# Performance work log

Hardware: AMD Instinct MI355X
Metric: run time of the kernel (lower is better)

Reference implementation:

```python
import jax, jax.numpy as jnp
import numpy as np

B, T, D, H, DFF, E = 4, 1024, 1024, 16, 4096, 8
DH = D // H
EPS = 1e-6


def setup_inputs() -> dict:
    key = jax.random.key(0)
    ks = jax.random.split(key, 16)
    s = 0.02
    return {
        "x": jax.random.normal(ks[0], (B, T, D), jnp.float32),
        "mask": jnp.ones((B, 1, 1, T), jnp.bool_),
        "Wq": jax.random.normal(ks[1], (D, D), jnp.float32) * s,
        "bq": jnp.zeros((D,), jnp.float32),
        "Wk": jax.random.normal(ks[2], (D, D), jnp.float32) * s,
        "bk": jnp.zeros((D,), jnp.float32),
        "Wv": jax.random.normal(ks[3], (D, D), jnp.float32) * s,
        "bv": jnp.zeros((D,), jnp.float32),
        "Wo": jax.random.normal(ks[4], (D, D), jnp.float32) * s,
        "bo": jnp.zeros((D,), jnp.float32),
        "ln1_a": jnp.ones((D,), jnp.float32),
        "ln1_b": jnp.zeros((D,), jnp.float32),
        "ln2_a": jnp.ones((D,), jnp.float32),
        "ln2_b": jnp.zeros((D,), jnp.float32),
        "gW": jax.random.normal(ks[5], (D, E), jnp.float32) * s,
        "gb": jnp.zeros((E,), jnp.float32),
        "W1": jax.random.normal(ks[6], (E, D, DFF), jnp.float32) * s,
        "b1": jnp.zeros((E, DFF), jnp.float32),
        "W2": jax.random.normal(ks[7], (E, DFF, D), jnp.float32) * s,
        "b2": jnp.zeros((E, D), jnp.float32),
    }


def layer_norm(x, a, b):
    # Faithful to source: torch std is unbiased (ddof=1), divides by (std + eps)
    mean = jnp.mean(x, -1, keepdims=True)
    std = jnp.std(x, -1, keepdims=True, ddof=1)
    return a * (x - mean) / (std + EPS) + b


def mha(x, mask, Wq, bq, Wk, bk, Wv, bv, Wo, bo):
    def split(h):
        return h.reshape(B, T, H, DH).transpose(0, 2, 1, 3)  # [B,H,T,DH]
    q = split(x @ Wq + bq)
    k = split(x @ Wk + bk)
    v = split(x @ Wv + bv)
    scores = jnp.einsum("bhqd,bhkd->bhqk", q, k) / jnp.sqrt(jnp.float32(DH))
    scores = jnp.where(mask, scores, jnp.float32(-1e9))
    attn = jax.nn.softmax(scores, axis=-1)
    out = jnp.einsum("bhqk,bhkd->bhqd", attn, v)
    out = out.transpose(0, 2, 1, 3).reshape(B, T, D)
    return out @ Wo + bo


def moe(xf, gW, gb, W1, b1, W2, b2):
    # xf: [N, D] flat tokens; top-1 Switch routing
    gate_probs = jax.nn.softmax(xf @ gW + gb, axis=-1)  # [N, E]
    top1_idx = jnp.argmax(gate_probs, axis=-1)          # [N]
    top1_p = jnp.max(gate_probs, axis=-1)               # [N]
    out = jnp.zeros_like(xf)
    for e in range(E):  # fixed small structural loop over experts
        h = jax.nn.relu(xf @ W1[e] + b1[e])
        oe = h @ W2[e] + b2[e]
        sel = (top1_idx == e).astype(xf.dtype)
        out = out + (sel * top1_p)[:, None] * oe
    counts = jax.nn.one_hot(top1_idx, E, dtype=jnp.float32).sum(0)
    aux_loss = jnp.sum((counts / (B * T)) ** 2) * E
    return out, aux_loss


def reference(x, mask, Wq, bq, Wk, bk, Wv, bv, Wo, bo,
              ln1_a, ln1_b, ln2_a, ln2_b, gW, gb, W1, b1, W2, b2):
    # sublayer[0]: x + attn(norm(x))  (dropout=0, inference)
    x1 = x + mha(layer_norm(x, ln1_a, ln1_b), mask, Wq, bq, Wk, bk, Wv, bv, Wo, bo)
    # MoE applied to x1 directly (source calls feed_forward(x), not on the norm)
    ff_out, aux_loss = moe(x1.reshape(-1, D), gW, gb, W1, b1, W2, b2)
    # sublayer[1] with lambda _: ff_out  -> x1 + ff_out (norm computed but discarded)
    x2 = x1 + ff_out.reshape(B, T, D)
    return x2, aux_loss
```

## Files before the change

### kernel.cpp

```cpp
#include <hip/hip_runtime.h>

#define DEV __device__ __forceinline__

typedef unsigned short u16;
typedef __bf16 bf16x8 __attribute__((ext_vector_type(8)));
typedef float f32x4 __attribute__((ext_vector_type(4)));
typedef unsigned short us8 __attribute__((ext_vector_type(8)));

static constexpr int Bn = 4, Tn = 1024, Dn = 1024, Hn = 16, DFFn = 4096, En = 8;
static constexpr int Nn = Bn * Tn;
static constexpr int MAXT = 40;
static constexpr int HROWS = 5120;

static constexpr int MT_E = 0, MT_P0 = 40, MCNT = 80, MCUR = 88, MSEG = 96, MPERM = 112;

static constexpr size_t WQKVT_O = 0;
static constexpr size_t WOT_O   = WQKVT_O + 3ull * 1024 * 1024 * 2;
static constexpr size_t W12T_O  = WOT_O + 1ull * 1024 * 1024 * 2;
static constexpr size_t X1F_O   = W12T_O + 8ull * 1024 * 4096 * 2;
static constexpr size_t XN_O    = X1F_O + (size_t)Nn * Dn * 4;
static constexpr size_t Q_O     = XN_O + (size_t)Nn * Dn * 2;
static constexpr size_t K_O     = Q_O + (size_t)Nn * Dn * 2;
static constexpr size_t VT_O    = K_O + (size_t)Nn * Dn * 2;
static constexpr size_t X1B_O   = VT_O + (size_t)Nn * Dn * 2;
static constexpr size_t P3_O    = XN_O;
static constexpr size_t H_O     = X1B_O + (size_t)Nn * Dn * 2;
static constexpr size_t TOPP_O  = H_O + (size_t)HROWS * DFFn * 2;
static constexpr size_t TIDX_O  = TOPP_O + (size_t)Nn * 4;
static constexpr size_t META_O  = TIDX_O + (size_t)Nn * 4;

DEV u16 f2bf(float f) {
  union { float f; unsigned u; } v; v.f = f;
  unsigned r = v.u + 0x7fffu + ((v.u >> 16) & 1u);
  return (u16)(r >> 16);
}
DEV float bf2f(u16 x) {
  union { unsigned u; float f; } v; v.u = ((unsigned)x) << 16;
  return v.f;
}

DEV void gload16(const void* g, void* l) {
  __builtin_amdgcn_global_load_lds(
      (__attribute__((address_space(1))) void*)(void*)g,
      (__attribute__((address_space(3))) void*)l, 16, 0, 0);
}

DEV void sdecode64(int o, int& row, int& c) {
  row = o >> 7;
  c = ((o >> 4) & 7) ^ (row & 7);
}

DEV int aswz(int r, int c) { return c ^ (r & 7) ^ (((r >> 3) & 3) << 1); }

__global__ __launch_bounds__(256) void tcast_kernel(
    const float* __restrict__ src, u16* __restrict__ dst,
    int R, int C, long srcBatch, long dstBatch) {
  __shared__ u16 tile[64][65];
  src += (long)blockIdx.z * srcBatch;
  dst += (long)blockIdx.z * dstBatch;
  int r0 = blockIdx.y * 64, c0 = blockIdx.x * 64;
  int tr = threadIdx.x >> 4;
  int tc = (threadIdx.x & 15) * 4;
#pragma unroll
  for (int i = 0; i < 4; i++) {
    int r = tr + i * 16;
    float4 v = *reinterpret_cast<const float4*>(&src[(long)(r0 + r) * C + c0 + tc]);
    tile[r][tc + 0] = f2bf(v.x); tile[r][tc + 1] = f2bf(v.y);
    tile[r][tc + 2] = f2bf(v.z); tile[r][tc + 3] = f2bf(v.w);
  }
  __syncthreads();
#pragma unroll
  for (int i = 0; i < 4; i++) {
    int r = tr + i * 16;
    ushort4 o;
    o.x = tile[tc + 0][r]; o.y = tile[tc + 1][r];
    o.z = tile[tc + 2][r]; o.w = tile[tc + 3][r];
    *reinterpret_cast<ushort4*>(&dst[(long)(c0 + r) * R + r0 + tc]) = o;
  }
}

__global__ __launch_bounds__(256) void ln_kernel(
    const float* __restrict__ x, const float* __restrict__ a,
    const float* __restrict__ b, u16* __restrict__ xn) {
  __shared__ float red[8];
  int row = blockIdx.x, tid = threadIdx.x;
  int lane = tid & 63, w = tid >> 6;
  float4 v = *reinterpret_cast<const float4*>(&x[(size_t)row * 1024 + tid * 4]);
  float s = v.x + v.y + v.z + v.w;
  float sq = v.x * v.x + v.y * v.y + v.z * v.z + v.w * v.w;
#pragma unroll
  for (int sh = 1; sh <= 32; sh <<= 1) { s += __shfl_xor(s, sh); sq += __shfl_xor(sq, sh); }
  if (lane == 0) { red[w] = s; red[4 + w] = sq; }
  __syncthreads();
  s = red[0] + red[1] + red[2] + red[3];
  sq = red[4] + red[5] + red[6] + red[7];
  float mean = s * (1.0f / 1024.0f);
  float var = (sq - s * mean) * (1.0f / 1023.0f);
  float inv = 1.0f / (sqrtf(var) + 1e-6f);
  float4 av = *reinterpret_cast<const float4*>(&a[tid * 4]);
  float4 bv = *reinterpret_cast<const float4*>(&b[tid * 4]);
  ushort4 o;
  o.x = f2bf(av.x * (v.x - mean) * inv + bv.x);
  o.y = f2bf(av.y * (v.y - mean) * inv + bv.y);
  o.z = f2bf(av.z * (v.z - mean) * inv + bv.z);
  o.w = f2bf(av.w * (v.w - mean) * inv + bv.w);
  *reinterpret_cast<ushort4*>(&xn[(size_t)row * 1024 + tid * 4]) = o;
}

template <int MODE, int BM, int NG, int KSPLIT>
__global__ __launch_bounds__(256, 3) void gemm3_k(
    const u16* __restrict__ Ag, const u16* __restrict__ Bg,
    const float* __restrict__ f0, const float* __restrict__ f1,
    const float* __restrict__ f2, const float* __restrict__ xres,
    float* __restrict__ x1f, u16* __restrict__ ob0, u16* __restrict__ ob1,
    u16* __restrict__ ob2, u16* __restrict__ pout, const int* __restrict__ meta) {
  constexpr int K = (MODE == 3) ? 4096 : 1024;
  constexpr int KS = K / KSPLIT;
  constexpr int NSUB = KS >> 6;
  constexpr int MT = (MODE <= 1) ? (4096 / BM) : MAXT;
  constexpr int NT = (MODE == 0) ? 24 : (MODE == 2) ? 32 : 8;
  constexpr int WR = BM / 2;
  constexpr int MI = WR / 16;
  constexpr int CA = BM / 32;

  __shared__ u16 As[BM * 64];
  __shared__ u16 Bs[128 * 64];

  const int tid = threadIdx.x, lane = tid & 63, w = tid >> 6;
  const int wm = w >> 1, wn = w & 1;
  const int cL = lane >> 4, rl15 = lane & 15;

  constexpr int NWG = MT * NT * KSPLIT;
  constexpr int q8 = NWG >> 3;
  int b = blockIdx.x;
  int lg = (b & 7) * q8 + (b >> 3);
  constexpr int PERG = KSPLIT * MT * NG;
  int g = lg / PERG, rem = lg - g * PERG;
  int s = rem / (MT * NG); rem -= s * (MT * NG);
  int mt = rem / NG;
  int nt = g * NG + (rem - (rem / NG) * NG);

  int m0 = mt * BM, n0 = nt * 128;
  const int k0 = s * KS;
  const u16* Abase = Ag;
  const u16* Bbase = Bg;
  int e = 0, cnt = 0, seg = 0, pos0 = 0;
  if (MODE >= 2) {
    e = meta[MT_E + mt];
    if (e < 0) return;
    cnt = meta[MCNT + e];
    seg = meta[MSEG + e];
    pos0 = meta[MT_P0 + mt];
    Bbase = Bg + (size_t)e * 4096 * 1024;
    if (MODE == 3) Abase = Ag + (size_t)(seg + pos0) * 4096;
    m0 = 0;
  }

  const u16* gA[CA];
  const u16* gB[4];
#pragma unroll
  for (int j = 0; j < CA; j++) {
    int row, c;
    sdecode64(j * 4096 + tid * 16, row, c);
    if constexpr (MODE == 2) {
      int pos = pos0 + row; if (pos >= cnt) pos = cnt - 1;
      int tok = meta[MPERM + seg + pos];
      gA[j] = Ag + (size_t)tok * 1024 + k0 + c * 8;
    } else {
      gA[j] = Abase + (size_t)(m0 + row) * K + k0 + c * 8;
    }
  }
#pragma unroll
  for (int j = 0; j < 4; j++) {
    int row, c;
    sdecode64(j * 4096 + tid * 16, row, c);
    gB[j] = Bbase + (size_t)(n0 + row) * K + k0 + c * 8;
  }

  auto STAGE = [&](int t) {
#pragma unroll
    for (int j = 0; j < CA; j++)
      gload16(gA[j] + t * 64, &As[j * 2048 + tid * 8]);
#pragma unroll
    for (int j = 0; j < 4; j++)
      gload16(gB[j] + t * 64, &Bs[j * 2048 + tid * 8]);
  };

  f32x4 acc[MI][4] = {};
  const char* Ab = reinterpret_cast<const char*>(&As[0]);
  const char* Bb = reinterpret_cast<const char*>(&Bs[0]);

  STAGE(0);
  for (int t = 0; t < NSUB; t++) {
    asm volatile("s_waitcnt vmcnt(0)" ::: "memory");
    __builtin_amdgcn_s_barrier();
#pragma unroll
    for (int ph = 0; ph < 2; ph++) {
      bf16x8 af[MI], bfr[4];
#pragma unroll
      for (int mi = 0; mi < MI; mi++) {
        int row = wm * WR + mi * 16 + rl15;
        af[mi] = *reinterpret_cast<const bf16x8*>(
            Ab + row * 128 + ((ph * 64 + cL * 16) ^ ((row & 7) << 4)));
      }
#pragma unroll
      for (int ni = 0; ni < 4; ni++) {
        int row = wn * 64 + ni * 16 + rl15;
        bfr[ni] = *reinterpret_cast<const bf16x8*>(
            Bb + row * 128 + ((ph * 64 + cL * 16) ^ ((row & 7) << 4)));
      }
#pragma unroll
      for (int mi = 0; mi < MI; mi++)
#pragma unroll
        for (int ni = 0; ni < 4; ni++)
          acc[mi][ni] = __builtin_amdgcn_mfma_f32_16x16x32_bf16(
              af[mi], bfr[ni], acc[mi][ni], 0, 0, 0);
    }
    __builtin_amdgcn_s_barrier();
    if (t + 1 < NSUB) STAGE(t + 1);
  }

  const int cl = rl15, rl = cL;
  if (MODE == 0) {
    int third = n0 >> 10;
    const float* bias = (third == 0) ? f0 : (third == 1) ? f1 : f2;
    const float qs = (third == 0) ? 0.125f : 1.0f;
#pragma unroll
    for (int ni = 0; ni < 4; ni++) {
      int col = n0 + wn * 64 + ni * 16 + cl;
      int jj = col & 1023;
      float bb_ = bias[jj];
      int hh = jj >> 6, dd = jj & 63;
#pragma unroll
      for (int mi = 0; mi < MI; mi++) {
        int t0 = m0 + wm * WR + mi * 16 + rl * 4;
        int b_ = t0 >> 10, tt = t0 & 1023;
        size_t bh = (size_t)(b_ * Hn + hh);
        if (third == 2) {
          ushort4 o4;
          o4.x = f2bf(acc[mi][ni][0] + bb_); o4.y = f2bf(acc[mi][ni][1] + bb_);
          o4.z = f2bf(acc[mi][ni][2] + bb_); o4.w = f2bf(acc[mi][ni][3] + bb_);
          *reinterpret_cast<ushort4*>(&ob2[(bh * 64 + dd) * 1024 + tt]) = o4;
        } else {
          u16* dst = (third == 0) ? ob0 : ob1;
#pragma unroll
          for (int r = 0; r < 4; r++)
            dst[(bh * 1024 + tt + r) * 64 + dd] = f2bf((acc[mi][ni][r] + bb_) * qs);
        }
      }
    }
  } else if (MODE == 1) {
#pragma unroll
    for (int ni = 0; ni < 4; ni++) {
      int col = n0 + wn * 64 + ni * 16 + cl;
      float bo_ = f0[col];
#pragma unroll
      for (int mi = 0; mi < MI; mi++) {
        int row = m0 + wm * WR + mi * 16 + rl * 4;
#pragma unroll
        for (int r = 0; r < 4; r++) {
          size_t idx = (size_t)(row + r) * 1024 + col;
          float v = acc[mi][ni][r] + bo_ + xres[idx];
          x1f[idx] = v;
          ob0[idx] = f2bf(v);
        }
      }
    }
  } else if (MODE == 2) {
#pragma unroll
    for (int ni = 0; ni < 4; ni++) {
      int col = n0 + wn * 64 + ni * 16 + cl;
      float b1_ = f0[(size_t)e * 4096 + col];
#pragma unroll
      for (int mi = 0; mi < MI; mi++) {
        int pos = pos0 + wm * WR + mi * 16 + rl * 4;
#pragma unroll
        for (int r = 0; r < 4; r++) {
          float v = acc[mi][ni][r] + b1_;
          v = v > 0.0f ? v : 0.0f;
          ob0[(size_t)(seg + pos + r) * 4096 + col] = f2bf(v);
        }
      }
    }
  } else {
#pragma unroll
    for (int ni = 0; ni < 4; ni++) {
      int col = n0 + wn * 64 + ni * 16 + cl;
#pragma unroll
      for (int mi = 0; mi < MI; mi++) {
        int pos = pos0 + wm * WR + mi * 16 + rl * 4;
#pragma unroll
        for (int r = 0; r < 4; r++)
          pout[((size_t)s * HROWS + seg + pos + r) * 1024 + col] = f2bf(acc[mi][ni][r]);
      }
    }
  }
}

__global__ __launch_bounds__(256) void reduce3_kernel(
    const u16* __restrict__ P3, const float* __restrict__ x1f,
    const float* __restrict__ topp, const float* __restrict__ b2,
    const int* __restrict__ meta, float* __restrict__ out) {
  int bidx = blockIdx.x;
  int tile = bidx >> 7, rowin = bidx & 127;
  int e = meta[MT_E + tile];
  if (e < 0) return;
  int cnt = meta[MCNT + e], seg = meta[MSEG + e];
  int pos = meta[MT_P0 + tile] + rowin;
  if (pos >= cnt) return;
  int tok = meta[MPERM + seg + pos];
  size_t prow = (size_t)(seg + pos) * 1024;
  float p = topp[tok];
  int c = threadIdx.x * 4;
  ushort4 u0 = *reinterpret_cast<const ushort4*>(&P3[prow + c]);
  ushort4 u1 = *reinterpret_cast<const ushort4*>(&P3[(size_t)HROWS * 1024 + prow + c]);
  float4 xr = *reinterpret_cast<const float4*>(&x1f[(size_t)tok * 1024 + c]);
  float4 bb = *reinterpret_cast<const float4*>(&b2[e * 1024 + c]);
  float4 o;
  o.x = xr.x + p * (bf2f(u0.x) + bf2f(u1.x) + bb.x);
  o.y = xr.y + p * (bf2f(u0.y) + bf2f(u1.y) + bb.y);
  o.z = xr.z + p * (bf2f(u0.z) + bf2f(u1.z) + bb.z);
  o.w = xr.w + p * (bf2f(u0.w) + bf2f(u1.w) + bb.w);
  *reinterpret_cast<float4*>(&out[(size_t)tok * 1024 + c]) = o;
}

__global__ __launch_bounds__(256, 4) void attn_kernel(
    const u16* __restrict__ q, const u16* __restrict__ k,
    const u16* __restrict__ vt, u16* __restrict__ attn) {
  __shared__ u16 Ks[2][64 * 64];
  __shared__ u16 Vs[2][64 * 64];
  const int tid = threadIdx.x, lane = tid & 63, w = tid >> 6;
  const int g = lane >> 4, l15 = lane & 15;

  int bb = blockIdx.x;
  int lg = (bb & 7) * 128 + (bb >> 3);
  const int bh = lg >> 4;
  const int qt = lg & 15;
  const size_t qkbase = (size_t)bh * Tn * 64;
  const size_t vtbase = (size_t)bh * 64 * Tn;
  const int qrow0 = qt * 64 + w * 16;

  bf16x8 qf[2];
  {
    const u16* qp = q + qkbase + (size_t)(qrow0 + l15) * 64 + g * 8;
    qf[0] = *reinterpret_cast<const bf16x8*>(qp);
    qf[1] = *reinterpret_cast<const bf16x8*>(qp + 32);
  }

  const u16* gk[2];
  const u16* gv[2];
#pragma unroll
  for (int j = 0; j < 2; j++) {
    int sidx = j * 256 + tid;
    int r = sidx >> 3, p = sidx & 7;
    int c = aswz(r, p);
    gk[j] = k + qkbase + (size_t)r * 64 + c * 8;
    gv[j] = vt + vtbase + (size_t)r * Tn + c * 8;
  }

  auto STAGE = [&](int t) {
    int buf = t & 1;
#pragma unroll
    for (int j = 0; j < 2; j++) {
      int sidx = j * 256 + tid;
      gload16(gk[j] + (size_t)t * 4096, &Ks[buf][sidx * 8]);
      gload16(gv[j] + (size_t)t * 64, &Vs[buf][sidx * 8]);
    }
  };

  f32x4 o[4] = {};
  float mrun = -1e30f, lsum = 0.0f;

  STAGE(0);
  for (int t = 0; t < 16; t++) {
    asm volatile("s_waitcnt vmcnt(0)" ::: "memory");
    __builtin_amdgcn_s_barrier();
    if (t + 1 < 16) STAGE(t + 1);

    const char* Kb = reinterpret_cast<const char*>(&Ks[t & 1][0]);
    const char* Vb = reinterpret_cast<const char*>(&Vs[t & 1][0]);

    f32x4 sk[2][2];
#pragma unroll
    for (int kb = 0; kb < 2; kb++)
#pragma unroll
      for (int m = 0; m < 2; m++) {
        f32x4 sa = {};
#pragma unroll
        for (int ph = 0; ph < 2; ph++) {
          int ksel = kb * 32 + (l15 >> 2) * 8 + m * 4 + (lane & 3);
          int pch = aswz(ksel, g + ph * 4);
          bf16x8 kf = *reinterpret_cast<const bf16x8*>(Kb + ksel * 128 + pch * 16);
          sa = __builtin_amdgcn_mfma_f32_16x16x32_bf16(kf, qf[ph], sa, 0, 0, 0);
        }
        sk[kb][m] = sa;
      }

    float mx = -1e30f;
#pragma unroll
    for (int kb = 0; kb < 2; kb++)
#pragma unroll
      for (int m = 0; m < 2; m++)
#pragma unroll
        for (int r = 0; r < 4; r++) mx = fmaxf(mx, sk[kb][m][r]);
    mx = fmaxf(mx, __shfl_xor(mx, 16));
    mx = fmaxf(mx, __shfl_xor(mx, 32));
    float mn = fmaxf(mrun, mx);
    float rsc = __expf(mrun - mn);
    mrun = mn;

    float pv[2][8];
    float ps = 0.0f;
#pragma unroll
    for (int kb = 0; kb < 2; kb++)
#pragma unroll
      for (int m = 0; m < 2; m++)
#pragma unroll
        for (int r = 0; r < 4; r++) {
          float pe = __expf(sk[kb][m][r] - mn);
          pv[kb][m * 4 + r] = pe;
          ps += pe;
        }
    ps += __shfl_xor(ps, 16);
    ps += __shfl_xor(ps, 32);
    lsum = lsum * rsc + ps;
#pragma unroll
    for (int nf = 0; nf < 4; nf++)
#pragma unroll
      for (int r = 0; r < 4; r++) o[nf][r] *= rsc;

    bf16x8 pf[2];
#pragma unroll
    for (int kb = 0; kb < 2; kb++)
#pragma unroll
      for (int j = 0; j < 8; j++) pf[kb][j] = (__bf16)pv[kb][j];

#pragma unroll
    for (int nf = 0; nf < 4; nf++) {
      int d = nf * 16 + l15;
#pragma unroll
      for (int kb = 0; kb < 2; kb++) {
        int pch = aswz(d, g + kb * 4);
        bf16x8 vf = *reinterpret_cast<const bf16x8*>(Vb + d * 128 + pch * 16);
        o[nf] = __builtin_amdgcn_mfma_f32_16x16x32_bf16(vf, pf[kb], o[nf], 0, 0, 0);
      }
    }
  }

  __syncthreads();
  u16* T = &Ks[0][0];
  float inv = 1.0f / lsum;
#pragma unroll
  for (int nf = 0; nf < 4; nf++)
#pragma unroll
    for (int r = 0; r < 4; r++) {
      int row = w * 16 + l15;
      int d = nf * 16 + g * 4 + r;
      int off = (row << 6) + ((((d >> 3) ^ (row & 7)) << 3) | (d & 7));
      T[off] = f2bf(o[nf][r] * inv);
    }
  __syncthreads();
  int b_ = bh >> 4, h_ = bh & 15;
#pragma unroll
  for (int p = 0; p < 2; p++) {
    int idx = p * 256 + tid;
    int row = idx >> 3, ch = idx & 7;
    int pch = ch ^ (row & 7);
    us8 v = *reinterpret_cast<const us8*>(T + (row << 6) + (pch << 3));
    *reinterpret_cast<us8*>(
        &attn[((size_t)(b_ * Tn + qt * 64 + row)) * 1024 + h_ * 64 + ch * 8]) = v;
  }
}

__global__ __launch_bounds__(256) void gate_kernel(
    const float* __restrict__ x1f, const float* __restrict__ gW,
    const float* __restrict__ gb, float* __restrict__ topp,
    int* __restrict__ tidx, int* __restrict__ meta) {
  int lane = threadIdx.x & 63;
  int n = blockIdx.x * 4 + (threadIdx.x >> 6);
  float acc[8] = {};
  const float* xr = x1f + (size_t)n * 1024;
  for (int kk = 0; kk < 16; kk++) {
    int kcol = kk * 64 + lane;
    float xv = xr[kcol];
    float4 g0 = *reinterpret_cast<const float4*>(&gW[kcol * 8]);
    float4 g1 = *reinterpret_cast<const float4*>(&gW[kcol * 8 + 4]);
    acc[0] = fmaf(xv, g0.x, acc[0]); acc[1] = fmaf(xv, g0.y, acc[1]);
    acc[2] = fmaf(xv, g0.z, acc[2]); acc[3] = fmaf(xv, g0.w, acc[3]);
    acc[4] = fmaf(xv, g1.x, acc[4]); acc[5] = fmaf(xv, g1.y, acc[5]);
    acc[6] = fmaf(xv, g1.z, acc[6]); acc[7] = fmaf(xv, g1.w, acc[7]);
  }
#pragma unroll
  for (int e2 = 0; e2 < 8; e2++)
#pragma unroll
    for (int sh = 1; sh <= 32; sh <<= 1) acc[e2] += __shfl_xor(acc[e2], sh);
  if (lane == 0) {
    float best = -1e30f; int bi = 0;
#pragma unroll
    for (int e2 = 0; e2 < 8; e2++) {
      float lgt = acc[e2] + gb[e2];
      if (lgt > best) { best = lgt; bi = e2; }
    }
    float den = 0.0f;
#pragma unroll
    for (int e2 = 0; e2 < 8; e2++) den += __expf(acc[e2] + gb[e2] - best);
    topp[n] = 1.0f / den;
    tidx[n] = bi;
    atomicAdd(&meta[MCNT + bi], 1);
  }
}

__global__ void scan_kernel(int* meta, float* aux_out) {
  if (threadIdx.x == 0) {
    int sb = 0, t = 0;
    float aux = 0.0f;
    for (int e2 = 0; e2 < 8; e2++) {
      meta[MSEG + e2] = sb;
      int c = meta[MCNT + e2];
      int ntile = (c + 127) >> 7;
      for (int i = 0; i < ntile; i++) { meta[MT_E + t] = e2; meta[MT_P0 + t] = i * 128; t++; }
      sb += ntile << 7;
      float fr = (float)c * (1.0f / 4096.0f);
      aux += fr * fr;
    }
    for (; t < MAXT; t++) { meta[MT_E + t] = -1; meta[MT_P0 + t] = 0; }
    aux_out[0] = aux * 8.0f;
  }
}

__global__ __launch_bounds__(256) void scatter_kernel(const int* __restrict__ tidx, int* meta) {
  int n = blockIdx.x * 256 + threadIdx.x;
  int e2 = tidx[n];
  int pos = atomicAdd(&meta[MCUR + e2], 1);
  meta[MPERM + meta[MSEG + e2] + pos] = n;
}

extern "C" void kernel_launch(void* const* d_in, const int* in_sizes, int n_in,
                              void* d_out, int out_size, void* d_ws, size_t ws_size,
                              hipStream_t stream) {
  const float* x   = (const float*)d_in[0];
  const float* Wq  = (const float*)d_in[2];
  const float* bq  = (const float*)d_in[3];
  const float* Wk  = (const float*)d_in[4];
  const float* bk  = (const float*)d_in[5];
  const float* Wv  = (const float*)d_in[6];
  const float* bv  = (const float*)d_in[7];
  const float* Wo  = (const float*)d_in[8];
  const float* bo  = (const float*)d_in[9];
  const float* ln1a = (const float*)d_in[10];
  const float* ln1b = (const float*)d_in[11];
  const float* gW  = (const float*)d_in[14];
  const float* gb  = (const float*)d_in[15];
  const float* W1  = (const float*)d_in[16];
  const float* b1  = (const float*)d_in[17];
  const float* W2  = (const float*)d_in[18];
  const float* b2  = (const float*)d_in[19];
  float* out = (float*)d_out;
  char* ws = (char*)d_ws;

  u16* wqkvt = (u16*)(ws + WQKVT_O);
  u16* wot   = (u16*)(ws + WOT_O);
  u16* w12t  = (u16*)(ws + W12T_O);
  u16* xn    = (u16*)(ws + XN_O);
  u16* qb    = (u16*)(ws + Q_O);
  u16* kb    = (u16*)(ws + K_O);
  u16* vtb   = (u16*)(ws + VT_O);
  float* x1f = (float*)(ws + X1F_O);
  u16* x1b   = (u16*)(ws + X1B_O);
  u16* p3    = (u16*)(ws + P3_O);
  u16* hb    = (u16*)(ws + H_O);
  float* topp = (float*)(ws + TOPP_O);
  int* tidx  = (int*)(ws + TIDX_O);
  int* meta  = (int*)(ws + META_O);

  hipMemsetAsync(meta + MCNT, 0, 16 * sizeof(int), stream);

  tcast_kernel<<<dim3(16, 16, 1), 256, 0, stream>>>(Wq, wqkvt, 1024, 1024, 0, 0);
  tcast_kernel<<<dim3(16, 16, 1), 256, 0, stream>>>(Wk, wqkvt + 1024 * 1024, 1024, 1024, 0, 0);
  tcast_kernel<<<dim3(16, 16, 1), 256, 0, stream>>>(Wv, wqkvt + 2 * 1024 * 1024, 1024, 1024, 0, 0);
  tcast_kernel<<<dim3(16, 16, 1), 256, 0, stream>>>(Wo, wot, 1024, 1024, 0, 0);
  tcast_kernel<<<dim3(64, 16, 8), 256, 0, stream>>>(W1, w12t, 1024, 4096,
                                                    (long)1024 * 4096, (long)4096 * 1024);

  ln_kernel<<<4096, 256, 0, stream>>>(x, ln1a, ln1b, xn);
  gemm3_k<0, 128, 4, 1><<<768, 256, 0, stream>>>(xn, wqkvt, bq, bk, bv, nullptr, nullptr,
                                                 qb, kb, vtb, nullptr, meta);
  attn_kernel<<<1024, 256, 0, stream>>>(qb, kb, vtb, xn);
  gemm3_k<1, 64, 4, 1><<<512, 256, 0, stream>>>(xn, wot, bo, nullptr, nullptr, x, x1f,
                                                x1b, nullptr, nullptr, nullptr, meta);
  gate_kernel<<<1024, 256, 0, stream>>>(x1f, gW, gb, topp, tidx, meta);
  scan_kernel<<<1, 64, 0, stream>>>(meta, out + (size_t)Nn * Dn);
  scatter_kernel<<<16, 256, 0, stream>>>(tidx, meta);
  gemm3_k<2, 128, 4, 1><<<1280, 256, 0, stream>>>(x1b, w12t, b1, nullptr, nullptr, nullptr,
                                                  nullptr, hb, nullptr, nullptr, nullptr, meta);
  tcast_kernel<<<dim3(16, 64, 8), 256, 0, stream>>>(W2, w12t, 4096, 1024,
                                                    (long)4096 * 1024, (long)1024 * 4096);
  gemm3_k<3, 128, 2, 2><<<640, 256, 0, stream>>>(hb, w12t, nullptr, nullptr, nullptr, nullptr,
                                                 nullptr, nullptr, nullptr, nullptr, p3, meta);
  reduce3_kernel<<<MAXT * 128, 256, 0, stream>>>(p3, x1f, topp, b2, meta, out);
}
```

Measured before the change: 379.8 us.

## Use 64-row M tiles in all GEMMs and merge the four weight casts

Hard-codes the GEMM M tile to 64 rows in every mode and raises launch bounds occupancy to 6, which doubles the grid sizes. The MoE expert GEMMs now use finer 64-row expert tiles, so each expert's padding is smaller. The scan kernel builds a second 64-row tile table next to the existing 128-row one, and the reduce kernel keeps using the 128-row table. The four Wq/Wk/Wv/Wo transpose-casts are folded into a single launch. The trade-off is less B-tile reuse per workgroup and more total B traffic, in exchange for better load balance and occupancy.

```diff
diff --git a/kernel.cpp b/kernel.cpp
--- a/kernel.cpp
+++ b/kernel.cpp
@@ -9,10 +9,13 @@
 
 static constexpr int Bn = 4, Tn = 1024, Dn = 1024, Hn = 16, DFFn = 4096, En = 8;
 static constexpr int Nn = Bn * Tn;
+static constexpr int MAXT64 = 72;
 static constexpr int MAXT = 40;
 static constexpr int HROWS = 5120;
 
-static constexpr int MT_E = 0, MT_P0 = 40, MCNT = 80, MCUR = 88, MSEG = 96, MPERM = 112;
+static constexpr int MT64_E = 0, MT64_P0 = 72;
+static constexpr int MT_E = 144, MT_P0 = 184;
+static constexpr int MCNT = 224, MCUR = 232, MSEG = 240, MPERM = 248;
 
 static constexpr size_t WQKVT_O = 0;
 static constexpr size_t WOT_O   = WQKVT_O + 3ull * 1024 * 1024 * 2;
@@ -51,6 +54,35 @@
 }
 
 DEV int aswz(int r, int c) { return c ^ (r & 7) ^ (((r >> 3) & 3) << 1); }
+
+__global__ __launch_bounds__(256) void tcast4_kernel(
+    const float* __restrict__ s0, const float* __restrict__ s1,
+    const float* __restrict__ s2, const float* __restrict__ s3,
+    u16* __restrict__ wqkvt, u16* __restrict__ wot) {
+  __shared__ u16 tile[64][65];
+  int z = blockIdx.z;
+  const float* src = (z == 0) ? s0 : (z == 1) ? s1 : (z == 2) ? s2 : s3;
+  u16* dst = (z < 3) ? wqkvt + (size_t)z * 1024 * 1024 : wot;
+  int r0 = blockIdx.y * 64, c0 = blockIdx.x * 64;
+  int tr = threadIdx.x >> 4;
+  int tc = (threadIdx.x & 15) * 4;
+#pragma unroll
+  for (int i = 0; i < 4; i++) {
+    int r = tr + i * 16;
+    float4 v = *reinterpret_cast<const float4*>(&src[(long)(r0 + r) * 1024 + c0 + tc]);
+    tile[r][tc + 0] = f2bf(v.x); tile[r][tc + 1] = f2bf(v.y);
+    tile[r][tc + 2] = f2bf(v.z); tile[r][tc + 3] = f2bf(v.w);
+  }
+  __syncthreads();
+#pragma unroll
+  for (int i = 0; i < 4; i++) {
+    int r = tr + i * 16;
+    ushort4 o;
+    o.x = tile[tc + 0][r]; o.y = tile[tc + 1][r];
+    o.z = tile[tc + 2][r]; o.w = tile[tc + 3][r];
+    *reinterpret_cast<ushort4*>(&dst[(long)(c0 + r) * 1024 + r0 + tc]) = o;
+  }
+}
 
 __global__ __launch_bounds__(256) void tcast_kernel(
     const float* __restrict__ src, u16* __restrict__ dst,
@@ -107,8 +139,8 @@
   *reinterpret_cast<ushort4*>(&xn[(size_t)row * 1024 + tid * 4]) = o;
 }
 
-template <int MODE, int BM, int NG, int KSPLIT>
-__global__ __launch_bounds__(256, 3) void gemm3_k(
+template <int MODE, int NG, int KSPLIT>
+__global__ __launch_bounds__(256, 6) void gemm3_k(
     const u16* __restrict__ Ag, const u16* __restrict__ Bg,
     const float* __restrict__ f0, const float* __restrict__ f1,
     const float* __restrict__ f2, const float* __restrict__ xres,
@@ -117,13 +149,13 @@
   constexpr int K = (MODE == 3) ? 4096 : 1024;
   constexpr int KS = K / KSPLIT;
   constexpr int NSUB = KS >> 6;
-  constexpr int MT = (MODE <= 1) ? (4096 / BM) : MAXT;
+  constexpr int MT = (MODE <= 1) ? 64 : MAXT64;
   constexpr int NT = (MODE == 0) ? 24 : (MODE == 2) ? 32 : 8;
-  constexpr int WR = BM / 2;
-  constexpr int MI = WR / 16;
-  constexpr int CA = BM / 32;
-
-  __shared__ u16 As[BM * 64];
+  constexpr int WR = 32;
+  constexpr int MI = 2;
+  constexpr int CA = 2;
+
+  __shared__ u16 As[64 * 64];
   __shared__ u16 Bs[128 * 64];
 
   const int tid = threadIdx.x, lane = tid & 63, w = tid >> 6;
@@ -140,17 +172,17 @@
   int mt = rem / NG;
   int nt = g * NG + (rem - (rem / NG) * NG);
 
-  int m0 = mt * BM, n0 = nt * 128;
+  int m0 = mt * 64, n0 = nt * 128;
   const int k0 = s * KS;
   const u16* Abase = Ag;
   const u16* Bbase = Bg;
   int e = 0, cnt = 0, seg = 0, pos0 = 0;
   if (MODE >= 2) {
-    e = meta[MT_E + mt];
+    e = meta[MT64_E + mt];
     if (e < 0) return;
     cnt = meta[MCNT + e];
     seg = meta[MSEG + e];
-    pos0 = meta[MT_P0 + mt];
+    pos0 = meta[MT64_P0 + mt];
     Bbase = Bg + (size_t)e * 4096 * 1024;
     if (MODE == 3) Abase = Ag + (size_t)(seg + pos0) * 4096;
     m0 = 0;
@@ -512,18 +544,21 @@
 
 __global__ void scan_kernel(int* meta, float* aux_out) {
   if (threadIdx.x == 0) {
-    int sb = 0, t = 0;
+    int sb = 0, t64 = 0, t1 = 0;
     float aux = 0.0f;
     for (int e2 = 0; e2 < 8; e2++) {
       meta[MSEG + e2] = sb;
       int c = meta[MCNT + e2];
-      int ntile = (c + 127) >> 7;
-      for (int i = 0; i < ntile; i++) { meta[MT_E + t] = e2; meta[MT_P0 + t] = i * 128; t++; }
-      sb += ntile << 7;
+      int n64 = (c + 63) >> 6;
+      for (int i = 0; i < n64; i++) { meta[MT64_E + t64] = e2; meta[MT64_P0 + t64] = i * 64; t64++; }
+      int n1 = (c + 127) >> 7;
+      for (int i = 0; i < n1; i++) { meta[MT_E + t1] = e2; meta[MT_P0 + t1] = i * 128; t1++; }
+      sb += n1 << 7;
       float fr = (float)c * (1.0f / 4096.0f);
       aux += fr * fr;
     }
-    for (; t < MAXT; t++) { meta[MT_E + t] = -1; meta[MT_P0 + t] = 0; }
+    for (; t64 < MAXT64; t64++) { meta[MT64_E + t64] = -1; meta[MT64_P0 + t64] = 0; }
+    for (; t1 < MAXT; t1++) { meta[MT_E + t1] = -1; meta[MT_P0 + t1] = 0; }
     aux_out[0] = aux * 8.0f;
   }
 }
@@ -575,27 +610,24 @@
 
   hipMemsetAsync(meta + MCNT, 0, 16 * sizeof(int), stream);
 
-  tcast_kernel<<<dim3(16, 16, 1), 256, 0, stream>>>(Wq, wqkvt, 1024, 1024, 0, 0);
-  tcast_kernel<<<dim3(16, 16, 1), 256, 0, stream>>>(Wk, wqkvt + 1024 * 1024, 1024, 1024, 0, 0);
-  tcast_kernel<<<dim3(16, 16, 1), 256, 0, stream>>>(Wv, wqkvt + 2 * 1024 * 1024, 1024, 1024, 0, 0);
-  tcast_kernel<<<dim3(16, 16, 1), 256, 0, stream>>>(Wo, wot, 1024, 1024, 0, 0);
+  tcast4_kernel<<<dim3(16, 16, 4), 256, 0, stream>>>(Wq, Wk, Wv, Wo, wqkvt, wot);
   tcast_kernel<<<dim3(64, 16, 8), 256, 0, stream>>>(W1, w12t, 1024, 4096,
                                                     (long)1024 * 4096, (long)4096 * 1024);
 
   ln_kernel<<<4096, 256, 0, stream>>>(x, ln1a, ln1b, xn);
-  gemm3_k<0, 128, 4, 1><<<768, 256, 0, stream>>>(xn, wqkvt, bq, bk, bv, nullptr, nullptr,
-                                                 qb, kb, vtb, nullptr, meta);
+  gemm3_k<0, 4, 1><<<1536, 256, 0, stream>>>(xn, wqkvt, bq, bk, bv, nullptr, nullptr,
+                                             qb, kb, vtb, nullptr, meta);
   attn_kernel<<<1024, 256, 0, stream>>>(qb, kb, vtb, xn);
-  gemm3_k<1, 64, 4, 1><<<512, 256, 0, stream>>>(xn, wot, bo, nullptr, nullptr, x, x1f,
-                                                x1b, nullptr, nullptr, nullptr, meta);
+  gemm3_k<1, 4, 1><<<512, 256, 0, stream>>>(xn, wot, bo, nullptr, nullptr, x, x1f,
+                                            x1b, nullptr, nullptr, nullptr, meta);
   gate_kernel<<<1024, 256, 0, stream>>>(x1f, gW, gb, topp, tidx, meta);
   scan_kernel<<<1, 64, 0, stream>>>(meta, out + (size_t)Nn * Dn);
   scatter_kernel<<<16, 256, 0, stream>>>(tidx, meta);
-  gemm3_k<2, 128, 4, 1><<<1280, 256, 0, stream>>>(x1b, w12t, b1, nullptr, nullptr, nullptr,
-                                                  nullptr, hb, nullptr, nullptr, nullptr, meta);
+  gemm3_k<2, 4, 1><<<2304, 256, 0, stream>>>(x1b, w12t, b1, nullptr, nullptr, nullptr,
+                                             nullptr, hb, nullptr, nullptr, nullptr, meta);
   tcast_kernel<<<dim3(16, 64, 8), 256, 0, stream>>>(W2, w12t, 4096, 1024,
                                                     (long)4096 * 1024, (long)1024 * 4096);
-  gemm3_k<3, 128, 2, 2><<<640, 256, 0, stream>>>(hb, w12t, nullptr, nullptr, nullptr, nullptr,
-                                                 nullptr, nullptr, nullptr, nullptr, p3, meta);
+  gemm3_k<3, 2, 2><<<1152, 256, 0, stream>>>(hb, w12t, nullptr, nullptr, nullptr, nullptr,
+                                             nullptr, nullptr, nullptr, nullptr, p3, meta);
   reduce3_kernel<<<MAXT * 128, 256, 0, stream>>>(p3, x1f, topp, b2, meta, out);
 }
```

Result: slower. 399.5 us (+5.2%).
